# Optimization experiments

Hardware: AMD Instinct MI355X
Metric: run time of the kernel (lower is better)

## Reference

```python
import jax, jax.numpy as jnp
import numpy as np

D_MODEL = 1024
NUM_HEADS = 16


def setup_inputs() -> dict:
    key = jax.random.key(0)
    ks = jax.random.split(key, 5)
    B, S, D = 4, 2048, D_MODEL
    std = (2.0 / (D + D)) ** 0.5
    x = jax.random.normal(ks[0], (B, S, D), dtype=jnp.float32)
    Wq = jax.random.normal(ks[1], (D, D), dtype=jnp.float32) * std
    Wk = jax.random.normal(ks[2], (D, D), dtype=jnp.float32) * std
    Wv = jax.random.normal(ks[3], (D, D), dtype=jnp.float32) * std
    Wo = jax.random.normal(ks[4], (D, D), dtype=jnp.float32) * std
    return {"x": x, "Wq": Wq, "Wk": Wk, "Wv": Wv, "Wo": Wo}


def reference(x, Wq, Wk, Wv, Wo):
    # x: [B, S, D]; W*: [out, in] applied as einsum('od,...d->...o')
    B, S, D = x.shape
    H = NUM_HEADS
    dk = D // H

    def split_heads(t):  # [B, S, D] -> [B, H, S, dk]
        return t.reshape(B, S, H, dk).transpose(0, 2, 1, 3)

    q = split_heads(jnp.einsum('od,bsd->bso', Wq, x))
    k = split_heads(jnp.einsum('od,bsd->bso', Wk, x))
    v = split_heads(jnp.einsum('od,bsd->bso', Wv, x))

    # materialized scores: [B, H, S, S]
    scores = jnp.einsum('bhqd,bhkd->bhqk', q, k) / jnp.sqrt(jnp.asarray(dk, x.dtype))
    causal = jnp.tril(jnp.ones((S, S), dtype=bool))  # query attends to keys <= query
    scores = jnp.where(causal, scores, -jnp.inf)
    attn = jax.nn.softmax(scores, axis=-1)
    out = jnp.einsum('bhqk,bhkd->bhqd', attn, v)  # [B, H, S, dk]
    out = out.transpose(0, 2, 1, 3).reshape(B, S, D)
    return jnp.einsum('od,bsd->bso', Wo, out)
```

## Files before the change

kernel.cpp:

```cpp
#include <hip/hip_runtime.h>
#include <math.h>

#define SEQ  2048
#define NBH  64
#define QT_N (SEQ/128)

typedef __bf16 bf16;
typedef float  f4v   __attribute__((ext_vector_type(4)));
typedef float  f32x4 __attribute__((ext_vector_type(4)));
typedef __bf16 bf16x8 __attribute__((ext_vector_type(8)));
typedef __bf16 bf16x4 __attribute__((ext_vector_type(4)));

typedef unsigned int u32g __attribute__((address_space(1)));
typedef unsigned int u32l __attribute__((address_space(3)));

__device__ __forceinline__ void async16(const void* g, void* l) {
    __builtin_amdgcn_global_load_lds((const u32g*)g, (u32l*)l, 16, 0, 0);
}

__global__ __launch_bounds__(256)
void castall(const float* __restrict__ x,  const float* __restrict__ wq,
             const float* __restrict__ wk, const float* __restrict__ wv,
             const float* __restrict__ wo, bf16* __restrict__ dst)
{
    const int i = (blockIdx.x * 256 + threadIdx.x) * 4;
    const float* s; int off; float sc = 1.f;
    if (i < 8388608)       { s = x;  off = 0; }
    else if (i < 9437184)  { s = wq; off = 8388608;  sc = 0.125f; }
    else if (i < 10485760) { s = wk; off = 9437184;  }
    else if (i < 11534336) { s = wv; off = 10485760; }
    else                   { s = wo; off = 11534336; }
    f4v v = *(const f4v*)&s[i - off];
    bf16x4 o;
    o[0] = (bf16)(v[0] * sc);
    o[1] = (bf16)(v[1] * sc);
    o[2] = (bf16)(v[2] * sc);
    o[3] = (bf16)(v[3] * sc);
    *(bf16x4*)&dst[i] = o;
}

template<int MODE>
__global__ __launch_bounds__(256)
void gemm_bf16(const bf16* __restrict__ A, const bf16* __restrict__ Bw,
               bf16* __restrict__ Oq, bf16* __restrict__ Ok, bf16* __restrict__ Ov,
               float* __restrict__ Of)
{
    __shared__ bf16 As[4096];
    __shared__ bf16 Bs[4096];

    const int t    = threadIdx.x;
    const int lane = t & 63;
    const int w    = t >> 6;
    const int m0   = blockIdx.y * 128;
    const int n0   = blockIdx.x * 128;
    const int wr   = (w >> 1) * 64;
    const int wc   = (w & 1) * 64;
    const int lr   = lane & 15;
    const int lk   = lane >> 4;

    f32x4 acc[4][4];
    #pragma unroll
    for (int i = 0; i < 4; ++i)
        #pragma unroll
        for (int j = 0; j < 4; ++j) acc[i][j] = f32x4{0.f, 0.f, 0.f, 0.f};

    int rowi[2], srcoff[2];
    #pragma unroll
    for (int it = 0; it < 2; ++it) {
        int b    = t * 16 + it * 4096;
        int row  = b >> 6;
        int koff = b & 63;
        rowi[it]   = row;
        srcoff[it] = (koff ^ (((row >> 1) & 3) << 4)) >> 1;
    }
    const bf16* Abase = A  + (size_t)m0 * 1024;
    const bf16* Bbase = Bw + (size_t)n0 * 1024;

    for (int k0 = 0; k0 < 1024; k0 += 32) {
        __syncthreads();
        #pragma unroll
        for (int it = 0; it < 2; ++it) {
            async16(Abase + (size_t)rowi[it] * 1024 + k0 + srcoff[it],
                    &As[w * 512 + it * 2048]);
            async16(Bbase + (size_t)rowi[it] * 1024 + k0 + srcoff[it],
                    &Bs[w * 512 + it * 2048]);
        }
        __syncthreads();

        bf16x8 af[4], bfr[4];
        #pragma unroll
        for (int mi = 0; mi < 4; ++mi) {
            int row = wr + mi * 16 + lr;
            af[mi] = *(const bf16x8*)((const char*)As + row * 64 +
                                      ((lk * 16) ^ (((row >> 1) & 3) << 4)));
        }
        #pragma unroll
        for (int ni = 0; ni < 4; ++ni) {
            int row = wc + ni * 16 + lr;
            bfr[ni] = *(const bf16x8*)((const char*)Bs + row * 64 +
                                       ((lk * 16) ^ (((row >> 1) & 3) << 4)));
        }
        #pragma unroll
        for (int mi = 0; mi < 4; ++mi)
            #pragma unroll
            for (int ni = 0; ni < 4; ++ni)
                acc[mi][ni] = __builtin_amdgcn_mfma_f32_16x16x32_bf16(
                    af[mi], bfr[ni], acc[mi][ni], 0, 0, 0);
    }

    #pragma unroll
    for (int mi = 0; mi < 4; ++mi) {
        #pragma unroll
        for (int r = 0; r < 4; ++r) {
            int m = m0 + wr + mi * 16 + lk * 4 + r;
            if (MODE == 0) {
                int bb = m >> 11, ss = m & 2047;
                #pragma unroll
                for (int ni = 0; ni < 4; ++ni) {
                    int n   = n0 + wc + ni * 16 + lr;
                    int mat = n >> 10;
                    int o   = n & 1023;
                    int hh  = o >> 6, dd = o & 63;
                    bf16* dst = (mat == 0) ? Oq : (mat == 1) ? Ok : Ov;
                    dst[(((size_t)(bb * 16 + hh)) * SEQ + ss) * 64 + dd] =
                        (bf16)acc[mi][ni][r];
                }
            } else {
                #pragma unroll
                for (int ni = 0; ni < 4; ++ni) {
                    int n = n0 + wc + ni * 16 + lr;
                    Of[(size_t)m * 1024 + n] = acc[mi][ni][r];
                }
            }
        }
    }
}

__global__ __launch_bounds__(256)
void vtrans(const bf16* __restrict__ V, bf16* __restrict__ Vt) {
    __shared__ bf16 ts[64][72];
    const int bh = blockIdx.y;
    const int st = blockIdx.x;
    const int t  = threadIdx.x;
    const int r  = t >> 3;
    const int c8 = (t & 7) * 8;

    #pragma unroll
    for (int it = 0; it < 2; ++it) {
        int row = r + it * 32;
        bf16x8 v = *(const bf16x8*)&V[((size_t)bh * SEQ + st * 64 + row) * 64 + c8];
        #pragma unroll
        for (int j = 0; j < 8; ++j) ts[c8 + j][row] = v[j];
    }
    __syncthreads();
    #pragma unroll
    for (int it = 0; it < 2; ++it) {
        int dk = r + it * 32;
        bf16x8 v = *(const bf16x8*)&ts[dk][c8];
        *(bf16x8*)&Vt[((size_t)bh * 64 + dk) * SEQ + st * 64 + c8] = v;
    }
}

__global__ __launch_bounds__(256)
void fattn(const bf16* __restrict__ Q, const bf16* __restrict__ K,
           const bf16* __restrict__ Vt, bf16* __restrict__ AO)
{
    __shared__ bf16 Ks[2][4096];
    __shared__ bf16 Vs[2][4096];
    __shared__ bf16 Ps[4][2048];

    const int pr   = blockIdx.x;
    const int bh   = blockIdx.y;
    const int t    = threadIdx.x;
    const int lane = t & 63;
    const int w    = t >> 6;
    const int lr   = lane & 15;
    const int lk   = lane >> 4;
    const int b    = bh >> 4, h = bh & 15;

    int rowi[2], srcoff[2];
    #pragma unroll
    for (int it = 0; it < 2; ++it) {
        int by   = t * 16 + it * 4096;
        int row  = by >> 7;
        int koff = by & 127;
        rowi[it]   = row;
        srcoff[it] = (koff ^ ((row & 7) << 4)) >> 1;
    }

    #pragma unroll 1
    for (int seg = 0; seg < 2; ++seg) {
        const int qt  = seg ? pr : (QT_N - 1 - pr);
        const int q0  = qt * 128 + w * 32;
        const int nkv = 2 * qt + 2;

        bf16x8 qf[2][2];
        #pragma unroll
        for (int mi = 0; mi < 2; ++mi)
            #pragma unroll
            for (int kc = 0; kc < 2; ++kc)
                qf[mi][kc] = *(const bf16x8*)
                    &Q[((size_t)bh * SEQ + q0 + mi * 16 + lr) * 64 + kc * 32 + lk * 8];

        f32x4 oacc[2][4];
        float m_[2][4], l_[2][4];
        #pragma unroll
        for (int mi = 0; mi < 2; ++mi)
            #pragma unroll
            for (int r = 0; r < 4; ++r) { m_[mi][r] = -3.0e38f; l_[mi][r] = 0.f; }
        #pragma unroll
        for (int mi = 0; mi < 2; ++mi)
            #pragma unroll
            for (int nd = 0; nd < 4; ++nd) oacc[mi][nd] = f32x4{0.f, 0.f, 0.f, 0.f};

        #pragma unroll
        for (int it = 0; it < 2; ++it) {
            async16(&K [((size_t)bh * SEQ + rowi[it]) * 64 + srcoff[it]],
                    &Ks[0][w * 512 + it * 2048]);
            async16(&Vt[((size_t)bh * 64 + rowi[it]) * SEQ + srcoff[it]],
                    &Vs[0][w * 512 + it * 2048]);
        }

        for (int kv = 0; kv < nkv; ++kv) {
            const int cur = kv & 1;
            if (kv + 1 < nkv) {
                const int nxt = cur ^ 1;
                #pragma unroll
                for (int it = 0; it < 2; ++it) {
                    async16(&K [((size_t)bh * SEQ + (kv + 1) * 64 + rowi[it]) * 64 + srcoff[it]],
                            &Ks[nxt][w * 512 + it * 2048]);
                    async16(&Vt[((size_t)bh * 64 + rowi[it]) * SEQ + (kv + 1) * 64 + srcoff[it]],
                            &Vs[nxt][w * 512 + it * 2048]);
                }
                asm volatile("s_waitcnt vmcnt(4)" ::: "memory");
            } else {
                asm volatile("s_waitcnt vmcnt(0)" ::: "memory");
            }
            __builtin_amdgcn_s_barrier();

            if (kv * 64 <= q0 + 31) {
                f32x4 sv[2][4];
                #pragma unroll
                for (int mi = 0; mi < 2; ++mi)
                    #pragma unroll
                    for (int ni = 0; ni < 4; ++ni) sv[mi][ni] = f32x4{0.f,0.f,0.f,0.f};
                __builtin_amdgcn_s_setprio(1);
                #pragma unroll
                for (int ni = 0; ni < 4; ++ni) {
                    #pragma unroll
                    for (int kc = 0; kc < 2; ++kc) {
                        int krow = ni * 16 + lr;
                        bf16x8 kf = *(const bf16x8*)((const char*)&Ks[cur][0] + krow * 128 +
                                    ((kc * 64 + lk * 16) ^ ((krow & 7) << 4)));
                        #pragma unroll
                        for (int mi = 0; mi < 2; ++mi)
                            sv[mi][ni] = __builtin_amdgcn_mfma_f32_16x16x32_bf16(
                                qf[mi][kc], kf, sv[mi][ni], 0, 0, 0);
                    }
                }
                __builtin_amdgcn_s_setprio(0);
                if (kv * 64 + 63 > q0) {
                    #pragma unroll
                    for (int mi = 0; mi < 2; ++mi)
                        #pragma unroll
                        for (int ni = 0; ni < 4; ++ni)
                            #pragma unroll
                            for (int r = 0; r < 4; ++r) {
                                int qg = q0 + mi * 16 + lk * 4 + r;
                                int kp = kv * 64 + ni * 16 + lr;
                                if (kp > qg) sv[mi][ni][r] = -3.0e38f;
                            }
                }
                #pragma unroll
                for (int mi = 0; mi < 2; ++mi) {
                    #pragma unroll
                    for (int r = 0; r < 4; ++r) {
                        float mx = fmaxf(fmaxf(sv[mi][0][r], sv[mi][1][r]),
                                         fmaxf(sv[mi][2][r], sv[mi][3][r]));
                        #pragma unroll
                        for (int off = 1; off < 16; off <<= 1)
                            mx = fmaxf(mx, __shfl_xor(mx, off));
                        float mn  = fmaxf(m_[mi][r], mx);
                        float fac = __expf(m_[mi][r] - mn);
                        m_[mi][r] = mn;
                        float ssum = 0.f;
                        int   prow  = mi * 16 + lk * 4 + r;
                        char* pbase = (char*)&Ps[w][0] + prow * 128;
                        #pragma unroll
                        for (int ni = 0; ni < 4; ++ni) {
                            float p = __expf(sv[mi][ni][r] - mn);
                            ssum += p;
                            int col2 = (ni * 16 + lr) * 2;
                            *(bf16*)(pbase + (col2 ^ ((prow & 7) << 4))) = (bf16)p;
                        }
                        #pragma unroll
                        for (int off = 1; off < 16; off <<= 1)
                            ssum += __shfl_xor(ssum, off);
                        l_[mi][r] = l_[mi][r] * fac + ssum;
                        #pragma unroll
                        for (int nd = 0; nd < 4; ++nd) oacc[mi][nd][r] *= fac;
                    }
                }
                __builtin_amdgcn_s_setprio(1);
                #pragma unroll
                for (int kc = 0; kc < 2; ++kc) {
                    bf16x8 pa[2];
                    #pragma unroll
                    for (int mi = 0; mi < 2; ++mi) {
                        int prow = mi * 16 + lr;
                        pa[mi] = *(const bf16x8*)((const char*)&Ps[w][0] + prow * 128 +
                                 ((kc * 64 + lk * 16) ^ ((prow & 7) << 4)));
                    }
                    #pragma unroll
                    for (int nd = 0; nd < 4; ++nd) {
                        int vrow = nd * 16 + lr;
                        bf16x8 vf = *(const bf16x8*)((const char*)&Vs[cur][0] + vrow * 128 +
                                    ((kc * 64 + lk * 16) ^ ((vrow & 7) << 4)));
                        #pragma unroll
                        for (int mi = 0; mi < 2; ++mi)
                            oacc[mi][nd] = __builtin_amdgcn_mfma_f32_16x16x32_bf16(
                                pa[mi], vf, oacc[mi][nd], 0, 0, 0);
                    }
                }
                __builtin_amdgcn_s_setprio(0);
            }
            __builtin_amdgcn_s_barrier();
        }

        #pragma unroll
        for (int mi = 0; mi < 2; ++mi)
            #pragma unroll
            for (int r = 0; r < 4; ++r) {
                int   srow = q0 + mi * 16 + lk * 4 + r;
                float rl   = 1.f / l_[mi][r];
                #pragma unroll
                for (int nd = 0; nd < 4; ++nd) {
                    int dk = nd * 16 + lr;
                    AO[((size_t)(b * SEQ + srow)) * 1024 + h * 64 + dk] =
                        (bf16)(oacc[mi][nd][r] * rl);
                }
            }
    }
}

extern "C" void kernel_launch(void* const* d_in, const int* in_sizes, int n_in,
                              void* d_out, int out_size, void* d_ws, size_t ws_size,
                              hipStream_t stream)
{
    const float* x  = (const float*)d_in[0];
    const float* Wq = (const float*)d_in[1];
    const float* Wk = (const float*)d_in[2];
    const float* Wv = (const float*)d_in[3];
    const float* Wo = (const float*)d_in[4];
    float* out = (float*)d_out;

    const size_t NE = (size_t)8192 * 1024;
    bf16* Xb    = (bf16*)d_ws;
    bf16* Wqkvb = Xb + NE;
    bf16* Wob   = Wqkvb + (size_t)3 * 1024 * 1024;
    bf16* Qb    = Wob   + (size_t)1024 * 1024;
    bf16* Kb    = Qb  + NE;
    bf16* Vb    = Kb  + NE;
    bf16* Vtb   = Vb  + NE;
    bf16* AOb   = Vtb + NE;

    castall<<<12288, 256, 0, stream>>>(x, Wq, Wk, Wv, Wo, Xb);

    dim3 g1(24, 64);
    gemm_bf16<0><<<g1, 256, 0, stream>>>(Xb, Wqkvb, Qb, Kb, Vb, nullptr);

    vtrans<<<dim3(32, 64), 256, 0, stream>>>(Vb, Vtb);

    fattn<<<dim3(8, NBH), 256, 0, stream>>>(Qb, Kb, Vtb, AOb);

    dim3 g3(8, 64);
    gemm_bf16<1><<<g3, 256, 0, stream>>>(AOb, Wob, nullptr, nullptr, nullptr, out);
}
```

Measured before the change: 316.8 us.

## Split attention work across 8 waves with lazy rescaling and exp2 softmax

```diff
diff --git a/kernel.cpp b/kernel.cpp
--- a/kernel.cpp
+++ b/kernel.cpp
@@ -26,7 +26,7 @@
     const int i = (blockIdx.x * 256 + threadIdx.x) * 4;
     const float* s; int off; float sc = 1.f;
     if (i < 8388608)       { s = x;  off = 0; }
-    else if (i < 9437184)  { s = wq; off = 8388608;  sc = 0.125f; }
+    else if (i < 9437184)  { s = wq; off = 8388608;  sc = 0.18033688011f; }
     else if (i < 10485760) { s = wk; off = 9437184;  }
     else if (i < 11534336) { s = wv; off = 10485760; }
     else                   { s = wo; off = 11534336; }
@@ -161,13 +161,13 @@
     }
 }
 
-__global__ __launch_bounds__(256)
+__global__ __launch_bounds__(512)
 void fattn(const bf16* __restrict__ Q, const bf16* __restrict__ K,
            const bf16* __restrict__ Vt, bf16* __restrict__ AO)
 {
     __shared__ bf16 Ks[2][4096];
     __shared__ bf16 Vs[2][4096];
-    __shared__ bf16 Ps[4][2048];
+    __shared__ bf16 Ps[8][1024];
 
     const int pr   = blockIdx.x;
     const int bh   = blockIdx.y;
@@ -178,72 +178,50 @@
     const int lk   = lane >> 4;
     const int b    = bh >> 4, h = bh & 15;
 
-    int rowi[2], srcoff[2];
-    #pragma unroll
-    for (int it = 0; it < 2; ++it) {
-        int by   = t * 16 + it * 4096;
-        int row  = by >> 7;
-        int koff = by & 127;
-        rowi[it]   = row;
-        srcoff[it] = (koff ^ ((row & 7) << 4)) >> 1;
-    }
+    const int by   = t * 16;
+    const int srow = by >> 7;
+    const int soff = ((by & 127) ^ ((srow & 7) << 4)) >> 1;
 
     #pragma unroll 1
     for (int seg = 0; seg < 2; ++seg) {
         const int qt  = seg ? pr : (QT_N - 1 - pr);
-        const int q0  = qt * 128 + w * 32;
+        const int q0  = qt * 128 + w * 16;
         const int nkv = 2 * qt + 2;
 
-        bf16x8 qf[2][2];
-        #pragma unroll
-        for (int mi = 0; mi < 2; ++mi)
-            #pragma unroll
-            for (int kc = 0; kc < 2; ++kc)
-                qf[mi][kc] = *(const bf16x8*)
-                    &Q[((size_t)bh * SEQ + q0 + mi * 16 + lr) * 64 + kc * 32 + lk * 8];
-
-        f32x4 oacc[2][4];
-        float m_[2][4], l_[2][4];
-        #pragma unroll
-        for (int mi = 0; mi < 2; ++mi)
-            #pragma unroll
-            for (int r = 0; r < 4; ++r) { m_[mi][r] = -3.0e38f; l_[mi][r] = 0.f; }
-        #pragma unroll
-        for (int mi = 0; mi < 2; ++mi)
-            #pragma unroll
-            for (int nd = 0; nd < 4; ++nd) oacc[mi][nd] = f32x4{0.f, 0.f, 0.f, 0.f};
-
-        #pragma unroll
-        for (int it = 0; it < 2; ++it) {
-            async16(&K [((size_t)bh * SEQ + rowi[it]) * 64 + srcoff[it]],
-                    &Ks[0][w * 512 + it * 2048]);
-            async16(&Vt[((size_t)bh * 64 + rowi[it]) * SEQ + srcoff[it]],
-                    &Vs[0][w * 512 + it * 2048]);
-        }
+        bf16x8 qf[2];
+        #pragma unroll
+        for (int kc = 0; kc < 2; ++kc)
+            qf[kc] = *(const bf16x8*)
+                &Q[((size_t)bh * SEQ + q0 + lr) * 64 + kc * 32 + lk * 8];
+
+        f32x4 oacc[4];
+        float m_[4], l_[4];
+        #pragma unroll
+        for (int r = 0; r < 4; ++r) { m_[r] = -3.0e38f; l_[r] = 0.f; }
+        #pragma unroll
+        for (int nd = 0; nd < 4; ++nd) oacc[nd] = f32x4{0.f, 0.f, 0.f, 0.f};
+
+        async16(&K [((size_t)bh * SEQ + srow) * 64 + soff], &Ks[0][w * 512]);
+        async16(&Vt[((size_t)bh * 64 + srow) * SEQ + soff], &Vs[0][w * 512]);
 
         for (int kv = 0; kv < nkv; ++kv) {
             const int cur = kv & 1;
             if (kv + 1 < nkv) {
                 const int nxt = cur ^ 1;
-                #pragma unroll
-                for (int it = 0; it < 2; ++it) {
-                    async16(&K [((size_t)bh * SEQ + (kv + 1) * 64 + rowi[it]) * 64 + srcoff[it]],
-                            &Ks[nxt][w * 512 + it * 2048]);
-                    async16(&Vt[((size_t)bh * 64 + rowi[it]) * SEQ + (kv + 1) * 64 + srcoff[it]],
-                            &Vs[nxt][w * 512 + it * 2048]);
-                }
-                asm volatile("s_waitcnt vmcnt(4)" ::: "memory");
+                async16(&K [((size_t)bh * SEQ + (kv + 1) * 64 + srow) * 64 + soff],
+                        &Ks[nxt][w * 512]);
+                async16(&Vt[((size_t)bh * 64 + srow) * SEQ + (kv + 1) * 64 + soff],
+                        &Vs[nxt][w * 512]);
+                asm volatile("s_waitcnt vmcnt(2)" ::: "memory");
             } else {
                 asm volatile("s_waitcnt vmcnt(0)" ::: "memory");
             }
             __builtin_amdgcn_s_barrier();
 
-            if (kv * 64 <= q0 + 31) {
-                f32x4 sv[2][4];
-                #pragma unroll
-                for (int mi = 0; mi < 2; ++mi)
-                    #pragma unroll
-                    for (int ni = 0; ni < 4; ++ni) sv[mi][ni] = f32x4{0.f,0.f,0.f,0.f};
+            if (kv * 64 <= q0 + 15) {
+                f32x4 sv[4];
+                #pragma unroll
+                for (int ni = 0; ni < 4; ++ni) sv[ni] = f32x4{0.f,0.f,0.f,0.f};
                 __builtin_amdgcn_s_setprio(1);
                 #pragma unroll
                 for (int ni = 0; ni < 4; ++ni) {
@@ -252,74 +230,73 @@
                         int krow = ni * 16 + lr;
                         bf16x8 kf = *(const bf16x8*)((const char*)&Ks[cur][0] + krow * 128 +
                                     ((kc * 64 + lk * 16) ^ ((krow & 7) << 4)));
-                        #pragma unroll
-                        for (int mi = 0; mi < 2; ++mi)
-                            sv[mi][ni] = __builtin_amdgcn_mfma_f32_16x16x32_bf16(
-                                qf[mi][kc], kf, sv[mi][ni], 0, 0, 0);
+                        sv[ni] = __builtin_amdgcn_mfma_f32_16x16x32_bf16(
+                            qf[kc], kf, sv[ni], 0, 0, 0);
                     }
                 }
                 __builtin_amdgcn_s_setprio(0);
                 if (kv * 64 + 63 > q0) {
                     #pragma unroll
-                    for (int mi = 0; mi < 2; ++mi)
+                    for (int ni = 0; ni < 4; ++ni)
                         #pragma unroll
-                        for (int ni = 0; ni < 4; ++ni)
-                            #pragma unroll
-                            for (int r = 0; r < 4; ++r) {
-                                int qg = q0 + mi * 16 + lk * 4 + r;
-                                int kp = kv * 64 + ni * 16 + lr;
-                                if (kp > qg) sv[mi][ni][r] = -3.0e38f;
-                            }
-                }
-                #pragma unroll
-                for (int mi = 0; mi < 2; ++mi) {
+                        for (int r = 0; r < 4; ++r) {
+                            int qg = q0 + lk * 4 + r;
+                            int kp = kv * 64 + ni * 16 + lr;
+                            if (kp > qg) sv[ni][r] = -3.0e38f;
+                        }
+                }
+                float mx[4];
+                bool need = false;
+                #pragma unroll
+                for (int r = 0; r < 4; ++r) {
+                    float m0 = fmaxf(fmaxf(sv[0][r], sv[1][r]),
+                                     fmaxf(sv[2][r], sv[3][r]));
+                    #pragma unroll
+                    for (int off = 1; off < 16; off <<= 1)
+                        m0 = fmaxf(m0, __shfl_xor(m0, off));
+                    mx[r] = m0;
+                    need = need || (m0 > m_[r] + 8.0f);
+                }
+                if (__ballot(need)) {
                     #pragma unroll
                     for (int r = 0; r < 4; ++r) {
-                        float mx = fmaxf(fmaxf(sv[mi][0][r], sv[mi][1][r]),
-                                         fmaxf(sv[mi][2][r], sv[mi][3][r]));
+                        float mn  = fmaxf(m_[r], mx[r]);
+                        float fac = exp2f(m_[r] - mn);
+                        m_[r] = mn;
+                        l_[r] *= fac;
                         #pragma unroll
-                        for (int off = 1; off < 16; off <<= 1)
-                            mx = fmaxf(mx, __shfl_xor(mx, off));
-                        float mn  = fmaxf(m_[mi][r], mx);
-                        float fac = __expf(m_[mi][r] - mn);
-                        m_[mi][r] = mn;
-                        float ssum = 0.f;
-                        int   prow  = mi * 16 + lk * 4 + r;
-                        char* pbase = (char*)&Ps[w][0] + prow * 128;
-                        #pragma unroll
-                        for (int ni = 0; ni < 4; ++ni) {
-                            float p = __expf(sv[mi][ni][r] - mn);
-                            ssum += p;
-                            int col2 = (ni * 16 + lr) * 2;
-                            *(bf16*)(pbase + (col2 ^ ((prow & 7) << 4))) = (bf16)p;
-                        }
-                        #pragma unroll
-                        for (int off = 1; off < 16; off <<= 1)
-                            ssum += __shfl_xor(ssum, off);
-                        l_[mi][r] = l_[mi][r] * fac + ssum;
-                        #pragma unroll
-                        for (int nd = 0; nd < 4; ++nd) oacc[mi][nd][r] *= fac;
+                        for (int nd = 0; nd < 4; ++nd) oacc[nd][r] *= fac;
                     }
                 }
+                #pragma unroll
+                for (int r = 0; r < 4; ++r) {
+                    float ssum = 0.f;
+                    int   prow  = lk * 4 + r;
+                    char* pbase = (char*)&Ps[w][0] + prow * 128;
+                    #pragma unroll
+                    for (int ni = 0; ni < 4; ++ni) {
+                        float p = exp2f(sv[ni][r] - m_[r]);
+                        ssum += p;
+                        int col2 = (ni * 16 + lr) * 2;
+                        *(bf16*)(pbase + (col2 ^ ((prow & 7) << 4))) = (bf16)p;
+                    }
+                    #pragma unroll
+                    for (int off = 1; off < 16; off <<= 1)
+                        ssum += __shfl_xor(ssum, off);
+                    l_[r] += ssum;
+                }
                 __builtin_amdgcn_s_setprio(1);
                 #pragma unroll
                 for (int kc = 0; kc < 2; ++kc) {
-                    bf16x8 pa[2];
-                    #pragma unroll
-                    for (int mi = 0; mi < 2; ++mi) {
-                        int prow = mi * 16 + lr;
-                        pa[mi] = *(const bf16x8*)((const char*)&Ps[w][0] + prow * 128 +
-                                 ((kc * 64 + lk * 16) ^ ((prow & 7) << 4)));
-                    }
+                    bf16x8 pa = *(const bf16x8*)((const char*)&Ps[w][0] + lr * 128 +
+                                ((kc * 64 + lk * 16) ^ ((lr & 7) << 4)));
                     #pragma unroll
                     for (int nd = 0; nd < 4; ++nd) {
                         int vrow = nd * 16 + lr;
                         bf16x8 vf = *(const bf16x8*)((const char*)&Vs[cur][0] + vrow * 128 +
                                     ((kc * 64 + lk * 16) ^ ((vrow & 7) << 4)));
-                        #pragma unroll
-                        for (int mi = 0; mi < 2; ++mi)
-                            oacc[mi][nd] = __builtin_amdgcn_mfma_f32_16x16x32_bf16(
-                                pa[mi], vf, oacc[mi][nd], 0, 0, 0);
+                        oacc[nd] = __builtin_amdgcn_mfma_f32_16x16x32_bf16(
+                            pa, vf, oacc[nd], 0, 0, 0);
                     }
                 }
                 __builtin_amdgcn_s_setprio(0);
@@ -328,18 +305,16 @@
         }
 
         #pragma unroll
-        for (int mi = 0; mi < 2; ++mi)
+        for (int r = 0; r < 4; ++r) {
+            int   srow2 = q0 + lk * 4 + r;
+            float rl    = 1.f / l_[r];
             #pragma unroll
-            for (int r = 0; r < 4; ++r) {
-                int   srow = q0 + mi * 16 + lk * 4 + r;
-                float rl   = 1.f / l_[mi][r];
-                #pragma unroll
-                for (int nd = 0; nd < 4; ++nd) {
-                    int dk = nd * 16 + lr;
-                    AO[((size_t)(b * SEQ + srow)) * 1024 + h * 64 + dk] =
-                        (bf16)(oacc[mi][nd][r] * rl);
-                }
+            for (int nd = 0; nd < 4; ++nd) {
+                int dk = nd * 16 + lr;
+                AO[((size_t)(b * SEQ + srow2)) * 1024 + h * 64 + dk] =
+                    (bf16)(oacc[nd][r] * rl);
             }
+        }
     }
 }
 
@@ -371,7 +346,7 @@
 
     vtrans<<<dim3(32, 64), 256, 0, stream>>>(Vb, Vtb);
 
-    fattn<<<dim3(8, NBH), 256, 0, stream>>>(Qb, Kb, Vtb, AOb);
+    fattn<<<dim3(8, NBH), 512, 0, stream>>>(Qb, Kb, Vtb, AOb);
 
     dim3 g3(8, 64);
     gemm_bf16<1><<<g3, 256, 0, stream>>>(AOb, Wob, nullptr, nullptr, nullptr, out);
```

New measurement: 308.1 us. 1.03x faster.
